# Performance work log

Hardware: AMD Instinct MI355X
Metric: run time of the kernel (lower is better)

Reference implementation:

```python
import jax, jax.numpy as jnp
import numpy as np

C = 1024
H = 16
T = 2048
B = 2
EPS = 1e-5


def _layernorm(x, g, b):
    mu = jnp.mean(x, axis=-1, keepdims=True)
    var = jnp.mean(jnp.square(x - mu), axis=-1, keepdims=True)
    return (x - mu) * jax.lax.rsqrt(var + EPS) * g + b


def setup_inputs() -> dict:
    key = jax.random.key(0)
    ks = jax.random.split(key, 12)
    s = 1.0 / np.sqrt(C)
    inp = {
        "x": jax.random.normal(ks[0], (B, T, C), jnp.float32),
        "ln1_g": jnp.ones((C,), jnp.float32),
        "ln1_b": jnp.zeros((C,), jnp.float32),
        "Wq": jax.random.normal(ks[1], (C, C), jnp.float32) * s,
        "bq": jnp.zeros((C,), jnp.float32),
        "Wk": jax.random.normal(ks[2], (C, C), jnp.float32) * s,
        "bk": jnp.zeros((C,), jnp.float32),
        "Wv": jax.random.normal(ks[3], (C, C), jnp.float32) * s,
        "bv": jnp.zeros((C,), jnp.float32),
        "Wp": jax.random.normal(ks[4], (C, C), jnp.float32) * s,
        "bp": jnp.zeros((C,), jnp.float32),
        "ln2_g": jnp.ones((C,), jnp.float32),
        "ln2_b": jnp.zeros((C,), jnp.float32),
        "W1": jax.random.normal(ks[5], (C, 4 * C), jnp.float32) * s,
        "b1": jnp.zeros((4 * C,), jnp.float32),
        "W2": jax.random.normal(ks[6], (4 * C, C), jnp.float32) * (1.0 / np.sqrt(4 * C)),
        "b2": jnp.zeros((C,), jnp.float32),
    }
    return inp


def _block(x, ln1_g, ln1_b, Wq, bq, Wk, bk, Wv, bv, Wp, bp,
           ln2_g, ln2_b, W1, b1, W2, b2):
    b, t, c = x.shape
    hd = c // H
    h = _layernorm(x, ln1_g, ln1_b)
    q = (h @ Wq + bq).reshape(b, t, H, hd).transpose(0, 2, 1, 3)  # [B,H,T,hd]
    k = (h @ Wk + bk).reshape(b, t, H, hd).transpose(0, 2, 1, 3)
    v = (h @ Wv + bv).reshape(b, t, H, hd).transpose(0, 2, 1, 3)
    att = jnp.einsum("bhqd,bhkd->bhqk", q, k) * (1.0 / np.sqrt(hd))
    causal = jnp.tril(jnp.ones((t, t), bool))
    att = jnp.where(causal, att, -jnp.inf)
    att = jax.nn.softmax(att, axis=-1)
    y = jnp.einsum("bhqk,bhkd->bhqd", att, v)
    y = y.transpose(0, 2, 1, 3).reshape(b, t, c)
    x = x + (y @ Wp + bp)
    h2 = _layernorm(x, ln2_g, ln2_b)
    m = jax.nn.gelu(h2 @ W1 + b1, approximate=False)  # torch nn.GELU default = exact
    x = x + (m @ W2 + b2)
    return x


def reference(x, ln1_g, ln1_b, Wq, bq, Wk, bk, Wv, bv, Wp, bp,
              ln2_g, ln2_b, W1, b1, W2, b2):
    return _block(x, ln1_g, ln1_b, Wq, bq, Wk, bk, Wv, bv, Wp, bp,
                  ln2_g, ln2_b, W1, b1, W2, b2)
```

## Files before the change

kernel.cpp:

```cpp
#include <hip/hip_runtime.h>
#include <hip/hip_bf16.h>


#define TT 2048
#define CC 1024

typedef __attribute__((ext_vector_type(8))) short short8;
typedef __attribute__((ext_vector_type(4))) float floatx4;

__device__ __forceinline__ unsigned short f2bf(float f) {
    union { float f; unsigned u; } x; x.f = f;
    unsigned r = x.u + 0x7fff + ((x.u >> 16) & 1);
    return (unsigned short)(r >> 16);
}

__device__ __forceinline__ float fast_exp2(float x) {
#if __has_builtin(__builtin_amdgcn_exp2f)
    return __builtin_amdgcn_exp2f(x);
#else
    return exp2f(x);
#endif
}

__device__ __forceinline__ float fast_rcp(float x) {
#if __has_builtin(__builtin_amdgcn_rcpf)
    return __builtin_amdgcn_rcpf(x);
#else
    return 1.0f / x;
#endif
}

__device__ __forceinline__ void gld_lds16(const unsigned short* g, unsigned short* l) {
    __builtin_amdgcn_global_load_lds(
        (const __attribute__((address_space(1))) unsigned int*)g,
        (__attribute__((address_space(3))) unsigned int*)l, 16, 0, 0);
}

__global__ __launch_bounds__(256)
void prep_weights(const float* __restrict__ Wq, const float* __restrict__ Wk,
                  const float* __restrict__ Wv, const float* __restrict__ Wp,
                  const float* __restrict__ W1, const float* __restrict__ W2,
                  const float* __restrict__ bq, const float* __restrict__ bk,
                  const float* __restrict__ bv,
                  __hip_bfloat16* __restrict__ wqkvT, __hip_bfloat16* __restrict__ wpT,
                  __hip_bfloat16* __restrict__ w1T, __hip_bfloat16* __restrict__ w2T,
                  float* __restrict__ bqkv) {
    __shared__ float tile[32][33];
    int bid = blockIdx.x;
    int tid = threadIdx.x;
    if (bid >= 12288) {
#pragma unroll
        for (int it = 0; it < 12; ++it) {
            int i = it * 256 + tid;
            bqkv[i] = (i < 1024) ? bq[i] : (i < 2048) ? bk[i - 1024] : bv[i - 2048];
        }
        return;
    }
    const float* src; __hip_bfloat16* dst; int K, N, bxi, byi;
    if (bid < 4096) {
        int w = bid >> 10;
        src = (w == 0) ? Wq : (w == 1) ? Wk : (w == 2) ? Wv : Wp;
        dst = (w == 3) ? wpT : wqkvT + (size_t)w * 1024 * 1024;
        K = 1024; N = 1024;
        int r = bid & 1023; bxi = r & 31; byi = r >> 5;
    } else if (bid < 8192) {
        src = W1; dst = w1T; K = 1024; N = 4096;
        int r = bid - 4096; bxi = r & 127; byi = r >> 7;
    } else {
        src = W2; dst = w2T; K = 4096; N = 1024;
        int r = bid - 8192; bxi = r & 31; byi = r >> 5;
    }
    int tx = tid & 31, ty = tid >> 5;
    int n0 = bxi * 32, k0 = byi * 32;
#pragma unroll
    for (int i = 0; i < 4; ++i)
        tile[ty + i * 8][tx] = src[(size_t)(k0 + ty + i * 8) * N + n0 + tx];
    __syncthreads();
#pragma unroll
    for (int i = 0; i < 4; ++i)
        dst[(size_t)(n0 + ty + i * 8) * K + k0 + tx] = __float2bfloat16(tile[tx][ty + i * 8]);
}

__global__ __launch_bounds__(256)
void ln_kernel(const float* __restrict__ x, const float* __restrict__ g,
               const float* __restrict__ b, __hip_bfloat16* __restrict__ out) {
    int row = blockIdx.x;
    int tid = threadIdx.x;
    const float* xr = x + (size_t)row * CC;
    float4 v = *(const float4*)(xr + tid * 4);
    float s = v.x + v.y + v.z + v.w;
#pragma unroll
    for (int m = 1; m < 64; m <<= 1) s += __shfl_xor(s, m, 64);
    __shared__ float red[4], red2[4];
    int wv = tid >> 6;
    if ((tid & 63) == 0) red[wv] = s;
    __syncthreads();
    float mu = (red[0] + red[1] + red[2] + red[3]) * (1.0f / CC);
    float d0 = v.x - mu, d1 = v.y - mu, d2 = v.z - mu, d3 = v.w - mu;
    float s2 = d0 * d0 + d1 * d1 + d2 * d2 + d3 * d3;
#pragma unroll
    for (int m = 1; m < 64; m <<= 1) s2 += __shfl_xor(s2, m, 64);
    if ((tid & 63) == 0) red2[wv] = s2;
    __syncthreads();
    float var = (red2[0] + red2[1] + red2[2] + red2[3]) * (1.0f / CC);
    float rs = rsqrtf(var + 1e-5f);
    float4 gv = *(const float4*)(g + tid * 4);
    float4 bv = *(const float4*)(b + tid * 4);
    __hip_bfloat16* o = out + (size_t)row * CC + tid * 4;
    o[0] = __float2bfloat16(d0 * rs * gv.x + bv.x);
    o[1] = __float2bfloat16(d1 * rs * gv.y + bv.y);
    o[2] = __float2bfloat16(d2 * rs * gv.z + bv.z);
    o[3] = __float2bfloat16(d3 * rs * gv.w + bv.w);
}

#define BM 128
#define BK 32

template <int MODE, int TBN>
__global__ __launch_bounds__(256)
void gemm_bt(const unsigned short* __restrict__ A, const unsigned short* __restrict__ Bt,
             const float* __restrict__ bias, const float* __restrict__ res,
             void* __restrict__ out, unsigned short* __restrict__ vt,
             int M, int N, int K) {
    constexpr int IM = (TBN == 64) ? 2 : 4;
    __shared__ __align__(16) unsigned short As[BM * BK];
    __shared__ __align__(16) unsigned short Bs[TBN * BK];
    int tid = threadIdx.x;
    int lane = tid & 63;
    int wave = tid >> 6;
    int wm = (TBN == 64) ? wave * 32 : (wave >> 1) * 64;
    int wn = (TBN == 64) ? 0 : (wave & 1) * 64;
    int rowBase = blockIdx.y * BM;
    int colBase = blockIdx.x * TBN;
    int lr = lane & 15;
    int quad = lane >> 4;
    int swz = (lr >> 1) & 3;
    int pA = (quad ^ swz) * 8;

    floatx4 acc[IM][4] = {};

    for (int k0 = 0; k0 < K; k0 += BK) {
#pragma unroll
        for (int hh = 0; hh < BM / 64; ++hh) {
            int s = tid + hh * 256;
            int r = s >> 2, p = s & 3;
            int c = p ^ ((r >> 1) & 3);
            gld_lds16(A + (size_t)(rowBase + r) * K + k0 + c * 8, As + (size_t)s * 8);
        }
#pragma unroll
        for (int hh = 0; hh < TBN / 64; ++hh) {
            int s = tid + hh * 256;
            int r = s >> 2, p = s & 3;
            int c = p ^ ((r >> 1) & 3);
            gld_lds16(Bt + (size_t)(colBase + r) * K + k0 + c * 8, Bs + (size_t)s * 8);
        }
        __syncthreads();
        short8 a[IM], b[4];
#pragma unroll
        for (int i = 0; i < IM; ++i)
            a[i] = *(const short8*)(As + (wm + i * 16 + lr) * BK + pA);
#pragma unroll
        for (int j = 0; j < 4; ++j)
            b[j] = *(const short8*)(Bs + (wn + j * 16 + lr) * BK + pA);
#pragma unroll
        for (int i = 0; i < IM; ++i)
#pragma unroll
            for (int j = 0; j < 4; ++j)
                acc[i][j] = __builtin_amdgcn_mfma_f32_16x16x32_bf16(a[i], b[j], acc[i][j], 0, 0, 0);
        __syncthreads();
    }

    if (MODE == 3 && colBase >= 2048) {
#pragma unroll
        for (int i = 0; i < IM; ++i) {
            int row0 = rowBase + wm + i * 16 + (lane >> 4) * 4;
            int bb = row0 >> 11, t0 = row0 & (TT - 1);
#pragma unroll
            for (int j = 0; j < 4; ++j) {
                int col = colBase + wn + j * 16 + (lane & 15);
                float bi = bias[col];
                int dg = col - 2048;
                int hh = dg >> 6, dd = dg & 63;
                ushort4 pk;
                pk.x = f2bf(acc[i][j][0] + bi);
                pk.y = f2bf(acc[i][j][1] + bi);
                pk.z = f2bf(acc[i][j][2] + bi);
                pk.w = f2bf(acc[i][j][3] + bi);
                *(ushort4*)(vt + ((size_t)(bb * 16 + hh) * 64 + dd) * TT + t0) = pk;
            }
        }
        return;
    }

    unsigned short* outb = (unsigned short*)out;
    float* outf = (float*)out;
#pragma unroll
    for (int i = 0; i < IM; ++i) {
        int row0 = rowBase + wm + i * 16 + (lane >> 4) * 4;
#pragma unroll
        for (int j = 0; j < 4; ++j) {
            int col = colBase + wn + j * 16 + (lane & 15);
            float bi = bias[col];
#pragma unroll
            for (int r = 0; r < 4; ++r) {
                size_t off = (size_t)(row0 + r) * N + col;
                float v = acc[i][j][r] + bi;
                if (MODE == 1) {
                    outf[off] = v + res[off];
                } else if (MODE == 2) {
                    outb[off] = f2bf(0.5f * v * (1.0f + erff(v * 0.70710678118f)));
                } else {
                    outb[off] = f2bf(v);
                }
            }
        }
    }
}

__global__ __launch_bounds__(256)
void attn_mfma(const unsigned short* __restrict__ qkv,
               const unsigned short* __restrict__ vT,
               unsigned short* __restrict__ y) {
    __shared__ __align__(16) unsigned short Plds[4][32 * 72];
    int wv = threadIdx.x >> 6, lane = threadIdx.x & 63;
    int quad = lane >> 4, l16 = lane & 15;
    int bx = blockIdx.x;
    int j = bx >> 5, bh = bx & 31;
    int qt = (wv == 0) ? j : (wv == 1) ? 31 - j : (wv == 2) ? 32 + j : 63 - j;
    int b = bh >> 4, h = bh & 15;

    const unsigned short* qb = qkv + (size_t)b * TT * 3072 + h * 64;
    const unsigned short* kb = qb + 1024;
    const unsigned short* vtb = vT + (size_t)bh * 64 * TT;
    unsigned short* Pw = Plds[wv];

    int q0 = qt * 32;
    short8 aq[2][2];
#pragma unroll
    for (int i = 0; i < 2; ++i)
#pragma unroll
        for (int c = 0; c < 2; ++c)
            aq[i][c] = *(const short8*)(qb + (size_t)(q0 + i * 16 + l16) * 3072 + c * 32 + quad * 8);

    short8 ones;
#pragma unroll
    for (int e = 0; e < 8; ++e) ones[e] = (short)0x3F80;

    floatx4 acc_o[2][4] = {};
    floatx4 lt[2] = {};

    const float k1 = 0.18033688f;
    const float k2 = 11.54156033f;

    int ktmax = (q0 + 31) >> 6;
    for (int kt = 0; kt <= ktmax; ++kt) {
        int k0 = kt * 64;
        short8 bk[4][2];
#pragma unroll
        for (int jt = 0; jt < 4; ++jt)
#pragma unroll
            for (int c = 0; c < 2; ++c)
                bk[jt][c] = *(const short8*)(kb + (size_t)(k0 + jt * 16 + l16) * 3072 + c * 32 + quad * 8);

        floatx4 sc[2][4] = {};
#pragma unroll
        for (int c = 0; c < 2; ++c)
#pragma unroll
            for (int i = 0; i < 2; ++i)
#pragma unroll
                for (int jt = 0; jt < 4; ++jt)
                    sc[i][jt] = __builtin_amdgcn_mfma_f32_16x16x32_bf16(aq[i][c], bk[jt][c], sc[i][jt], 0, 0, 0);

        if (kt == ktmax) {
#pragma unroll
            for (int i = 0; i < 2; ++i)
#pragma unroll
                for (int jt = 0; jt < 4; ++jt)
#pragma unroll
                    for (int r = 0; r < 4; ++r)
                        if (k0 + jt * 16 + l16 > q0 + i * 16 + quad * 4 + r) sc[i][jt][r] = -3.0e38f;
        }

#pragma unroll
        for (int i = 0; i < 2; ++i)
#pragma unroll
            for (int r = 0; r < 4; ++r) {
                int qrow = i * 16 + quad * 4 + r;
#pragma unroll
                for (int jt = 0; jt < 4; ++jt) {
                    float p = fast_exp2(fmaf(sc[i][jt][r], k1, -k2));
                    Pw[qrow * 72 + jt * 16 + l16] =
                        (unsigned short)(__float_as_uint(p) >> 16);
                }
            }

#pragma unroll
        for (int c = 0; c < 2; ++c) {
            short8 bv4[4];
#pragma unroll
            for (int jd = 0; jd < 4; ++jd)
                bv4[jd] = *(const short8*)(vtb + (size_t)(jd * 16 + l16) * TT + k0 + c * 32 + quad * 8);
#pragma unroll
            for (int i = 0; i < 2; ++i) {
                short8 ap = *(const short8*)(Pw + (i * 16 + l16) * 72 + c * 32 + quad * 8);
                lt[i] = __builtin_amdgcn_mfma_f32_16x16x32_bf16(ap, ones, lt[i], 0, 0, 0);
#pragma unroll
                for (int jd = 0; jd < 4; ++jd)
                    acc_o[i][jd] = __builtin_amdgcn_mfma_f32_16x16x32_bf16(ap, bv4[jd], acc_o[i][jd], 0, 0, 0);
            }
        }
    }

#pragma unroll
    for (int i = 0; i < 2; ++i)
#pragma unroll
        for (int r = 0; r < 4; ++r) {
            float rl = fast_rcp(lt[i][r]);
            int row = b * TT + q0 + i * 16 + quad * 4 + r;
#pragma unroll
            for (int jd = 0; jd < 4; ++jd)
                y[(size_t)row * CC + h * 64 + jd * 16 + l16] = f2bf(acc_o[i][jd][r] * rl);
        }
}

extern "C" void kernel_launch(void* const* d_in, const int* in_sizes, int n_in,
                              void* d_out, int out_size, void* d_ws, size_t ws_size,
                              hipStream_t stream) {
    const float* x    = (const float*)d_in[0];
    const float* ln1g = (const float*)d_in[1];
    const float* ln1b = (const float*)d_in[2];
    const float* Wq   = (const float*)d_in[3];
    const float* bq   = (const float*)d_in[4];
    const float* Wk   = (const float*)d_in[5];
    const float* bk   = (const float*)d_in[6];
    const float* Wv   = (const float*)d_in[7];
    const float* bv   = (const float*)d_in[8];
    const float* Wp   = (const float*)d_in[9];
    const float* bp   = (const float*)d_in[10];
    const float* ln2g = (const float*)d_in[11];
    const float* ln2b = (const float*)d_in[12];
    const float* W1   = (const float*)d_in[13];
    const float* b1   = (const float*)d_in[14];
    const float* W2   = (const float*)d_in[15];
    const float* b2   = (const float*)d_in[16];

    const int M = 2 * TT;
    char* ws = (char*)d_ws;
    size_t off = 0;
    auto alloc = [&](size_t bytes) {
        char* p = ws + off;
        off += (bytes + 255) & ~(size_t)255;
        return p;
    };
    __hip_bfloat16* hb    = (__hip_bfloat16*)alloc((size_t)M * CC * 2);
    __hip_bfloat16* h2b   = (__hip_bfloat16*)alloc((size_t)M * CC * 2);
    unsigned short* yb    = (unsigned short*)alloc((size_t)M * CC * 2);
    __hip_bfloat16* wqkvT = (__hip_bfloat16*)alloc((size_t)3072 * CC * 2);
    __hip_bfloat16* wpT   = (__hip_bfloat16*)alloc((size_t)CC * CC * 2);
    __hip_bfloat16* w1T   = (__hip_bfloat16*)alloc((size_t)4096 * CC * 2);
    __hip_bfloat16* w2T   = (__hip_bfloat16*)alloc((size_t)CC * 4096 * 2);
    float*          bqkv  = (float*)alloc(3072 * 4);
    float*          x2    = (float*)alloc((size_t)M * CC * 4);
    unsigned short* qkv   = (unsigned short*)alloc((size_t)M * 3072 * 2);
    unsigned short* vT    = (unsigned short*)alloc((size_t)32 * 64 * TT * 2);
    unsigned short* mb    = (unsigned short*)alloc((size_t)M * 4096 * 2);
    (void)ws_size; (void)in_sizes; (void)n_in; (void)out_size;

    dim3 tb(256);
    prep_weights<<<12289, tb, 0, stream>>>(Wq, Wk, Wv, Wp, W1, W2, bq, bk, bv,
                                           wqkvT, wpT, w1T, w2T, bqkv);

    ln_kernel<<<M, 256, 0, stream>>>(x, ln1g, ln1b, hb);
    gemm_bt<3, 128><<<dim3(3072 / 128, M / BM), tb, 0, stream>>>(
        (const unsigned short*)hb, (const unsigned short*)wqkvT, bqkv, nullptr, qkv, vT, M, 3072, 1024);
    attn_mfma<<<512, tb, 0, stream>>>(qkv, vT, yb);
    gemm_bt<1, 64><<<dim3(1024 / 64, M / BM), tb, 0, stream>>>(
        yb, (const unsigned short*)wpT, bp, x, x2, nullptr, M, 1024, 1024);
    ln_kernel<<<M, 256, 0, stream>>>(x2, ln2g, ln2b, h2b);
    gemm_bt<2, 128><<<dim3(4096 / 128, M / BM), tb, 0, stream>>>(
        (const unsigned short*)h2b, (const unsigned short*)w1T, b1, nullptr, mb, nullptr, M, 4096, 1024);
    gemm_bt<1, 64><<<dim3(1024 / 64, M / BM), tb, 0, stream>>>(
        mb, (const unsigned short*)w2T, b2, x2, (float*)d_out, nullptr, M, 1024, 4096);
}
```

Before: 427.0 us.

## Prefetch next K/V tiles in registers and remap query tiles to contiguous segments

The attention kernel now loads the next K and V tiles into registers while the MFMAs run on the current tile, so global-load latency overlaps with compute. It also changes how query tiles are assigned: each block's four waves take four adjacent query tiles, with the heaviest segments launched first, replacing the earlier mirrored pairing that balanced causal work within a block. The prefetch raises VGPR pressure and can cut occupancy, and the new mapping can leave waves within a block with unequal work.

```diff
diff --git a/kernel.cpp b/kernel.cpp
--- a/kernel.cpp
+++ b/kernel.cpp
@@ -225,8 +225,8 @@
     int wv = threadIdx.x >> 6, lane = threadIdx.x & 63;
     int quad = lane >> 4, l16 = lane & 15;
     int bx = blockIdx.x;
-    int j = bx >> 5, bh = bx & 31;
-    int qt = (wv == 0) ? j : (wv == 1) ? 31 - j : (wv == 2) ? 32 + j : 63 - j;
+    int seg = bx >> 5, bh = bx & 31;
+    int qt = (15 - seg) * 4 + wv;
     int b = bh >> 4, h = bh & 15;
 
     const unsigned short* qb = qkv + (size_t)b * TT * 3072 + h * 64;
@@ -252,15 +252,32 @@
     const float k1 = 0.18033688f;
     const float k2 = 11.54156033f;
 
+    auto loadK = [&](int k0, short8 (&dk)[4][2]) {
+#pragma unroll
+        for (int jt = 0; jt < 4; ++jt)
+#pragma unroll
+            for (int c = 0; c < 2; ++c)
+                dk[jt][c] = *(const short8*)(kb + (size_t)(k0 + jt * 16 + l16) * 3072 + c * 32 + quad * 8);
+    };
+    auto loadV = [&](int k0, short8 (&dv)[2][4]) {
+#pragma unroll
+        for (int c = 0; c < 2; ++c)
+#pragma unroll
+            for (int jd = 0; jd < 4; ++jd)
+                dv[c][jd] = *(const short8*)(vtb + (size_t)(jd * 16 + l16) * TT + k0 + c * 32 + quad * 8);
+    };
+
     int ktmax = (q0 + 31) >> 6;
+    short8 ck[4][2], cv[2][4];
+    loadK(0, ck);
+    loadV(0, cv);
+
     for (int kt = 0; kt <= ktmax; ++kt) {
         int k0 = kt * 64;
-        short8 bk[4][2];
-#pragma unroll
-        for (int jt = 0; jt < 4; ++jt)
-#pragma unroll
-            for (int c = 0; c < 2; ++c)
-                bk[jt][c] = *(const short8*)(kb + (size_t)(k0 + jt * 16 + l16) * 3072 + c * 32 + quad * 8);
+        int kp = (kt < ktmax) ? (k0 + 64) : k0;
+        short8 nk[4][2], nv[2][4];
+        loadK(kp, nk);
+        loadV(kp, nv);
 
         floatx4 sc[2][4] = {};
 #pragma unroll
@@ -269,7 +286,7 @@
             for (int i = 0; i < 2; ++i)
 #pragma unroll
                 for (int jt = 0; jt < 4; ++jt)
-                    sc[i][jt] = __builtin_amdgcn_mfma_f32_16x16x32_bf16(aq[i][c], bk[jt][c], sc[i][jt], 0, 0, 0);
+                    sc[i][jt] = __builtin_amdgcn_mfma_f32_16x16x32_bf16(aq[i][c], ck[jt][c], sc[i][jt], 0, 0, 0);
 
         if (kt == ktmax) {
 #pragma unroll
@@ -296,19 +313,26 @@
 
 #pragma unroll
         for (int c = 0; c < 2; ++c) {
-            short8 bv4[4];
-#pragma unroll
-            for (int jd = 0; jd < 4; ++jd)
-                bv4[jd] = *(const short8*)(vtb + (size_t)(jd * 16 + l16) * TT + k0 + c * 32 + quad * 8);
 #pragma unroll
             for (int i = 0; i < 2; ++i) {
                 short8 ap = *(const short8*)(Pw + (i * 16 + l16) * 72 + c * 32 + quad * 8);
                 lt[i] = __builtin_amdgcn_mfma_f32_16x16x32_bf16(ap, ones, lt[i], 0, 0, 0);
 #pragma unroll
                 for (int jd = 0; jd < 4; ++jd)
-                    acc_o[i][jd] = __builtin_amdgcn_mfma_f32_16x16x32_bf16(ap, bv4[jd], acc_o[i][jd], 0, 0, 0);
+                    acc_o[i][jd] = __builtin_amdgcn_mfma_f32_16x16x32_bf16(ap, cv[c][jd], acc_o[i][jd], 0, 0, 0);
             }
         }
+
+#pragma unroll
+        for (int jt = 0; jt < 4; ++jt)
+#pragma unroll
+            for (int c = 0; c < 2; ++c)
+                ck[jt][c] = nk[jt][c];
+#pragma unroll
+        for (int c = 0; c < 2; ++c)
+#pragma unroll
+            for (int jd = 0; jd < 4; ++jd)
+                cv[c][jd] = nv[c][jd];
     }
 
 #pragma unroll
```

Result: slower. 441.8 us (+3.5%).

## Split attention KV range across wave pairs and merge partial sums in LDS

Applied to the files above, without the earlier changes.

Attention now assigns two query tiles per block, each handled by two waves that split the causal key-tile range in half, doubling the grid to 1024 blocks. The second wave writes its partial output and row-sum to shared memory, and the first adds them before normalising. This aims to shorten the per-wave critical path and improve load balance and occupancy. The cost is extra LDS, two block barriers and a reduction step. The split is safe without max-subtraction because the exponent uses a fixed offset.

```diff
diff --git a/kernel.cpp b/kernel.cpp
--- a/kernel.cpp
+++ b/kernel.cpp
@@ -222,11 +222,14 @@
                const unsigned short* __restrict__ vT,
                unsigned short* __restrict__ y) {
     __shared__ __align__(16) unsigned short Plds[4][32 * 72];
+    __shared__ __align__(16) float cbuf[2][32][66];
+    __shared__ float cltb[2][32];
     int wv = threadIdx.x >> 6, lane = threadIdx.x & 63;
     int quad = lane >> 4, l16 = lane & 15;
     int bx = blockIdx.x;
-    int j = bx >> 5, bh = bx & 31;
-    int qt = (wv == 0) ? j : (wv == 1) ? 31 - j : (wv == 2) ? 32 + j : 63 - j;
+    int u = bx >> 5, bh = bx & 31;
+    int t = wv >> 1, s = wv & 1;
+    int qt = (31 - u) * 2 + t;
     int b = bh >> 4, h = bh & 15;
 
     const unsigned short* qb = qkv + (size_t)b * TT * 3072 + h * 64;
@@ -252,15 +255,19 @@
     const float k1 = 0.18033688f;
     const float k2 = 11.54156033f;
 
-    int ktmax = (q0 + 31) >> 6;
-    for (int kt = 0; kt <= ktmax; ++kt) {
+    int ntile = (qt >> 1) + 1;
+    int nhalf = ntile >> 1;
+    int ktbeg = s ? nhalf : 0;
+    int ktend = s ? ntile : nhalf;
+
+    for (int kt = ktbeg; kt < ktend; ++kt) {
         int k0 = kt * 64;
-        short8 bk[4][2];
+        short8 ck[4][2];
 #pragma unroll
         for (int jt = 0; jt < 4; ++jt)
 #pragma unroll
             for (int c = 0; c < 2; ++c)
-                bk[jt][c] = *(const short8*)(kb + (size_t)(k0 + jt * 16 + l16) * 3072 + c * 32 + quad * 8);
+                ck[jt][c] = *(const short8*)(kb + (size_t)(k0 + jt * 16 + l16) * 3072 + c * 32 + quad * 8);
 
         floatx4 sc[2][4] = {};
 #pragma unroll
@@ -269,9 +276,9 @@
             for (int i = 0; i < 2; ++i)
 #pragma unroll
                 for (int jt = 0; jt < 4; ++jt)
-                    sc[i][jt] = __builtin_amdgcn_mfma_f32_16x16x32_bf16(aq[i][c], bk[jt][c], sc[i][jt], 0, 0, 0);
-
-        if (kt == ktmax) {
+                    sc[i][jt] = __builtin_amdgcn_mfma_f32_16x16x32_bf16(aq[i][c], ck[jt][c], sc[i][jt], 0, 0, 0);
+
+        if (kt == ntile - 1) {
 #pragma unroll
             for (int i = 0; i < 2; ++i)
 #pragma unroll
@@ -296,31 +303,51 @@
 
 #pragma unroll
         for (int c = 0; c < 2; ++c) {
-            short8 bv4[4];
+            short8 cv[4];
 #pragma unroll
             for (int jd = 0; jd < 4; ++jd)
-                bv4[jd] = *(const short8*)(vtb + (size_t)(jd * 16 + l16) * TT + k0 + c * 32 + quad * 8);
+                cv[jd] = *(const short8*)(vtb + (size_t)(jd * 16 + l16) * TT + k0 + c * 32 + quad * 8);
 #pragma unroll
             for (int i = 0; i < 2; ++i) {
                 short8 ap = *(const short8*)(Pw + (i * 16 + l16) * 72 + c * 32 + quad * 8);
                 lt[i] = __builtin_amdgcn_mfma_f32_16x16x32_bf16(ap, ones, lt[i], 0, 0, 0);
 #pragma unroll
                 for (int jd = 0; jd < 4; ++jd)
-                    acc_o[i][jd] = __builtin_amdgcn_mfma_f32_16x16x32_bf16(ap, bv4[jd], acc_o[i][jd], 0, 0, 0);
-            }
-        }
-    }
-
-#pragma unroll
-    for (int i = 0; i < 2; ++i)
-#pragma unroll
-        for (int r = 0; r < 4; ++r) {
-            float rl = fast_rcp(lt[i][r]);
-            int row = b * TT + q0 + i * 16 + quad * 4 + r;
-#pragma unroll
-            for (int jd = 0; jd < 4; ++jd)
-                y[(size_t)row * CC + h * 64 + jd * 16 + l16] = f2bf(acc_o[i][jd][r] * rl);
-        }
+                    acc_o[i][jd] = __builtin_amdgcn_mfma_f32_16x16x32_bf16(ap, cv[jd], acc_o[i][jd], 0, 0, 0);
+            }
+        }
+    }
+
+    __syncthreads();
+    if (s) {
+#pragma unroll
+        for (int i = 0; i < 2; ++i)
+#pragma unroll
+            for (int r = 0; r < 4; ++r) {
+                int row = i * 16 + quad * 4 + r;
+#pragma unroll
+                for (int jd = 0; jd < 4; ++jd)
+                    cbuf[t][row][jd * 16 + l16] = acc_o[i][jd][r];
+                if (l16 == 0) cltb[t][row] = lt[i][r];
+            }
+    }
+    __syncthreads();
+    if (!s) {
+#pragma unroll
+        for (int i = 0; i < 2; ++i)
+#pragma unroll
+            for (int r = 0; r < 4; ++r) {
+                int row = i * 16 + quad * 4 + r;
+                float l2 = lt[i][r] + cltb[t][row];
+                float rl = fast_rcp(l2);
+                int grow = b * TT + q0 + row;
+#pragma unroll
+                for (int jd = 0; jd < 4; ++jd) {
+                    float v = acc_o[i][jd][r] + cbuf[t][row][jd * 16 + l16];
+                    y[(size_t)grow * CC + h * 64 + jd * 16 + l16] = f2bf(v * rl);
+                }
+            }
+    }
 }
 
 extern "C" void kernel_launch(void* const* d_in, const int* in_sizes, int n_in,
@@ -373,7 +400,7 @@
     ln_kernel<<<M, 256, 0, stream>>>(x, ln1g, ln1b, hb);
     gemm_bt<3, 128><<<dim3(3072 / 128, M / BM), tb, 0, stream>>>(
         (const unsigned short*)hb, (const unsigned short*)wqkvT, bqkv, nullptr, qkv, vT, M, 3072, 1024);
-    attn_mfma<<<512, tb, 0, stream>>>(qkv, vT, yb);
+    attn_mfma<<<1024, tb, 0, stream>>>(qkv, vT, yb);
     gemm_bt<1, 64><<<dim3(1024 / 64, M / BM), tb, 0, stream>>>(
         yb, (const unsigned short*)wpT, bp, x, x2, nullptr, M, 1024, 1024);
     ln_kernel<<<M, 256, 0, stream>>>(x2, ln2g, ln2b, h2b);
```

After: 420.7 us. No clear change (-1.5%).
